# Performance work log

Hardware: AMD Instinct MI355X
Metric: run time of the kernel (lower is better)

## Reference

```python
import math
import jax, jax.numpy as jnp
import numpy as np

B, H, S, D = 2, 16, 2048, 64

def setup_inputs() -> dict:
    key = jax.random.key(0)
    kq, kk, kv, km = jax.random.split(key, 4)
    q = jax.random.normal(kq, (B, H, S, D), dtype=jnp.float32)
    k = jax.random.normal(kk, (B, H, S, D), dtype=jnp.float32)
    v = jax.random.normal(kv, (B, H, S, D), dtype=jnp.float32)
    mask = jax.random.randint(km, (B, S, S), 0, 2, dtype=jnp.int32)
    return {"q": q, "k": k, "v": v, "mask": mask}

def reference(q, k, v, mask):
    # attn = q @ (k^T / sqrt(d))  -> [B,H,Sq,Sk]
    scale = 1.0 / math.sqrt(q.shape[-1])
    attn = jnp.einsum("bhqd,bhkd->bhqk", q, k * scale)
    # masked_fill where mask.unsqueeze(1) == 1
    attn = jnp.where(mask[:, None, :, :] == 1, jnp.float32(-1e9), attn)
    attn = jax.nn.softmax(attn, axis=-1)
    # dropout is identity in eval / p=0
    res = jnp.einsum("bhqk,bhkd->bhqd", attn, v)
    return (res, attn)
```

## Files before the change

### kernel.cpp

```cpp
#include <hip/hip_runtime.h>

#define B_ 2
#define H_ 16
#define S_ 2048
#define D_ 64
#define QB 64
#define KT 64
#define NTHREADS 512

typedef _Float16 f16;
typedef _Float16 f16x8 __attribute__((ext_vector_type(8)));
typedef _Float16 f16x4 __attribute__((ext_vector_type(4)));
typedef _Float16 f16x2 __attribute__((ext_vector_type(2)));
typedef float f32x4 __attribute__((ext_vector_type(4)));

#define MFMA16(a, b, c) __builtin_amdgcn_mfma_f32_16x16x32_f16(a, b, c, 0, 0, 0)

__global__ __launch_bounds__(NTHREADS)
void attn_kernel(const float* __restrict__ q, const float* __restrict__ k,
                 const float* __restrict__ v, const int* __restrict__ mask,
                 float* __restrict__ out)
{
    __shared__ f16 Qsh[QB][D_ + 8];
    __shared__ f16 Ksh[KT][D_ + 8];
    __shared__ f16 Vsh[KT][D_ + 2];
    __shared__ f16 Psh[QB][KT + 8];
    __shared__ float rowred[QB];
    __shared__ float rlsh[QB];

    const int tid  = threadIdx.x;
    const int wave = tid >> 6;
    const int lane = tid & 63;
    const int quad = lane >> 4;
    const int l16  = lane & 15;
    const int qi   = wave & 3;
    const int ni   = wave >> 2;

    const int qb = blockIdx.x;
    const int h  = blockIdx.y;
    const int b  = blockIdx.z;
    const int bh = b * H_ + h;

    const float* Qg = q + ((size_t)bh * S_ + (size_t)qb * QB) * D_;
    const float* Kg = k + (size_t)bh * S_ * D_;
    const float* Vg = v + (size_t)bh * S_ * D_;
    const int*   Mg = mask + ((size_t)b * S_ + (size_t)qb * QB) * S_;
    float* res_out  = out + ((size_t)bh * S_ + (size_t)qb * QB) * D_;
    float* attn_out = out + (size_t)B_ * H_ * S_ * D_
                          + ((size_t)bh * S_ + (size_t)qb * QB) * S_;

    if (tid < QB) rowred[tid] = 0.f;

    {
        const int row = tid >> 3;
        const int c   = (tid & 7) * 8;
        const float4 q0 = *(const float4*)(Qg + row * D_ + c);
        const float4 q1 = *(const float4*)(Qg + row * D_ + c + 4);
        f16x8 o;
        o[0] = (f16)(q0.x * 0.125f); o[1] = (f16)(q0.y * 0.125f);
        o[2] = (f16)(q0.z * 0.125f); o[3] = (f16)(q0.w * 0.125f);
        o[4] = (f16)(q1.x * 0.125f); o[5] = (f16)(q1.y * 0.125f);
        o[6] = (f16)(q1.z * 0.125f); o[7] = (f16)(q1.w * 0.125f);
        *(f16x8*)&Qsh[row][c] = o;
    }
    __syncthreads();

    const int qrow0 = qi * 16 + quad * 4;
    const f16x8 a0 = *(const f16x8*)&Qsh[qi * 16 + l16][quad * 8];
    const f16x8 a1 = *(const f16x8*)&Qsh[qi * 16 + l16][32 + quad * 8];

    const int colbase = ni * 16 + l16;
    const int* mp0 = Mg + (size_t)qrow0 * S_ + colbase;

    const int skk = tid >> 3;
    const int sd0 = (tid & 7) * 8;

    float psum[4] = {0.f, 0.f, 0.f, 0.f};
    for (int kt = 0; kt < S_ / KT; ++kt) {
        {
            const float* src = Kg + ((size_t)(kt * KT + skk)) * D_ + sd0;
            const float4 x0 = *(const float4*)(src);
            const float4 x1 = *(const float4*)(src + 4);
            f16x8 o;
            o[0] = (f16)x0.x; o[1] = (f16)x0.y; o[2] = (f16)x0.z; o[3] = (f16)x0.w;
            o[4] = (f16)x1.x; o[5] = (f16)x1.y; o[6] = (f16)x1.z; o[7] = (f16)x1.w;
            *(f16x8*)&Ksh[skk][sd0] = o;
        }
        __syncthreads();
        const f16x8 b0a = *(const f16x8*)&Ksh[colbase][quad * 8];
        const f16x8 b0b = *(const f16x8*)&Ksh[colbase][32 + quad * 8];
        const f16x8 b1a = *(const f16x8*)&Ksh[32 + colbase][quad * 8];
        const f16x8 b1b = *(const f16x8*)&Ksh[32 + colbase][32 + quad * 8];
        f32x4 c0 = {0.f, 0.f, 0.f, 0.f};
        c0 = MFMA16(a0, b0a, c0);
        c0 = MFMA16(a1, b0b, c0);
        f32x4 c1 = {0.f, 0.f, 0.f, 0.f};
        c1 = MFMA16(a0, b1a, c1);
        c1 = MFMA16(a1, b1b, c1);
        const int* mp = mp0 + kt * KT;
#pragma unroll
        for (int r = 0; r < 4; ++r) {
            const int m0 = mp[(size_t)r * S_];
            const int m1 = mp[(size_t)r * S_ + 32];
            psum[r] += (m0 == 1) ? 0.f : __expf(c0[r]);
            psum[r] += (m1 == 1) ? 0.f : __expf(c1[r]);
        }
        __syncthreads();
    }

#pragma unroll
    for (int r = 0; r < 4; ++r) {
        psum[r] += __shfl_xor(psum[r], 1);
        psum[r] += __shfl_xor(psum[r], 2);
        psum[r] += __shfl_xor(psum[r], 4);
        psum[r] += __shfl_xor(psum[r], 8);
    }
    if (l16 == 0) {
#pragma unroll
        for (int r = 0; r < 4; ++r) atomicAdd(&rowred[qrow0 + r], psum[r]);
    }
    __syncthreads();
    if (tid < QB) rlsh[tid] = 1.0f / rowred[tid];
    __syncthreads();
    float rlq[4];
#pragma unroll
    for (int r = 0; r < 4; ++r) rlq[r] = rlsh[qrow0 + r];

    f32x4 oaccA = {0.f, 0.f, 0.f, 0.f};
    f32x4 oaccB = {0.f, 0.f, 0.f, 0.f};
    float* ap0 = attn_out + (size_t)qrow0 * S_ + colbase;

    for (int kt = 0; kt < S_ / KT; ++kt) {
        {
            const float* srck = Kg + ((size_t)(kt * KT + skk)) * D_ + sd0;
            const float4 x0 = *(const float4*)(srck);
            const float4 x1 = *(const float4*)(srck + 4);
            f16x8 o;
            o[0] = (f16)x0.x; o[1] = (f16)x0.y; o[2] = (f16)x0.z; o[3] = (f16)x0.w;
            o[4] = (f16)x1.x; o[5] = (f16)x1.y; o[6] = (f16)x1.z; o[7] = (f16)x1.w;
            *(f16x8*)&Ksh[skk][sd0] = o;

            const float* srcv = Vg + ((size_t)(kt * KT + skk)) * D_ + sd0;
            const float4 y0 = *(const float4*)(srcv);
            const float4 y1 = *(const float4*)(srcv + 4);
            f16x2 p01, p23, p45, p67;
            p01[0] = (f16)y0.x; p01[1] = (f16)y0.y;
            p23[0] = (f16)y0.z; p23[1] = (f16)y0.w;
            p45[0] = (f16)y1.x; p45[1] = (f16)y1.y;
            p67[0] = (f16)y1.z; p67[1] = (f16)y1.w;
            *(f16x2*)&Vsh[skk][sd0]     = p01;
            *(f16x2*)&Vsh[skk][sd0 + 2] = p23;
            *(f16x2*)&Vsh[skk][sd0 + 4] = p45;
            *(f16x2*)&Vsh[skk][sd0 + 6] = p67;
        }
        __syncthreads();
        const f16x8 b0a = *(const f16x8*)&Ksh[colbase][quad * 8];
        const f16x8 b0b = *(const f16x8*)&Ksh[colbase][32 + quad * 8];
        const f16x8 b1a = *(const f16x8*)&Ksh[32 + colbase][quad * 8];
        const f16x8 b1b = *(const f16x8*)&Ksh[32 + colbase][32 + quad * 8];
        f32x4 c0 = {0.f, 0.f, 0.f, 0.f};
        c0 = MFMA16(a0, b0a, c0);
        c0 = MFMA16(a1, b0b, c0);
        f32x4 c1 = {0.f, 0.f, 0.f, 0.f};
        c1 = MFMA16(a0, b1a, c1);
        c1 = MFMA16(a1, b1b, c1);
        const int* mp = mp0 + kt * KT;
        float* ap = ap0 + kt * KT;
#pragma unroll
        for (int r = 0; r < 4; ++r) {
            const int m0 = mp[(size_t)r * S_];
            const int m1 = mp[(size_t)r * S_ + 32];
            const float e0 = (m0 == 1) ? 0.f : __expf(c0[r]);
            const float e1 = (m1 == 1) ? 0.f : __expf(c1[r]);
            const float p0 = e0 * rlq[r];
            const float p1 = e1 * rlq[r];
            ap[(size_t)r * S_]      = p0;
            ap[(size_t)r * S_ + 32] = p1;
            Psh[qrow0 + r][colbase]      = (f16)p0;
            Psh[qrow0 + r][colbase + 32] = (f16)p1;
        }
        __syncthreads();
        const f16x8 pa0 = *(const f16x8*)&Psh[qi * 16 + l16][quad * 8];
        const f16x8 pa1 = *(const f16x8*)&Psh[qi * 16 + l16][32 + quad * 8];
        f16x8 vb0a, vb1a, vb0b, vb1b;
        const int dcolA = colbase;
        const int dcolB = colbase + 32;
#pragma unroll
        for (int j = 0; j < 8; ++j) {
            vb0a[j] = Vsh[quad * 8 + j][dcolA];
            vb1a[j] = Vsh[32 + quad * 8 + j][dcolA];
            vb0b[j] = Vsh[quad * 8 + j][dcolB];
            vb1b[j] = Vsh[32 + quad * 8 + j][dcolB];
        }
        oaccA = MFMA16(pa0, vb0a, oaccA);
        oaccA = MFMA16(pa1, vb1a, oaccA);
        oaccB = MFMA16(pa0, vb0b, oaccB);
        oaccB = MFMA16(pa1, vb1b, oaccB);
        __syncthreads();
    }

#pragma unroll
    for (int r = 0; r < 4; ++r) {
        res_out[(size_t)(qrow0 + r) * D_ + colbase]      = oaccA[r];
        res_out[(size_t)(qrow0 + r) * D_ + colbase + 32] = oaccB[r];
    }
}

extern "C" void kernel_launch(void* const* d_in, const int* in_sizes, int n_in,
                              void* d_out, int out_size, void* d_ws, size_t ws_size,
                              hipStream_t stream) {
    (void)in_sizes; (void)n_in; (void)out_size; (void)d_ws; (void)ws_size;
    const float* q   = (const float*)d_in[0];
    const float* k   = (const float*)d_in[1];
    const float* v   = (const float*)d_in[2];
    const int*  mask = (const int*)d_in[3];
    float* out = (float*)d_out;
    dim3 grid(S_ / QB, H_, B_);
    attn_kernel<<<grid, dim3(NTHREADS), 0, stream>>>(q, k, v, mask, out);
}
```

Baseline: 836.7 us.

## Prefetch next K/V tile and mask into registers during compute

```diff
diff --git a/kernel.cpp b/kernel.cpp
--- a/kernel.cpp
+++ b/kernel.cpp
@@ -6,25 +6,33 @@
 #define D_ 64
 #define QB 64
 #define KT 64
+#define NT (S_ / KT)
 #define NTHREADS 512
+#define KP 4
 
 typedef _Float16 f16;
 typedef _Float16 f16x8 __attribute__((ext_vector_type(8)));
-typedef _Float16 f16x4 __attribute__((ext_vector_type(4)));
 typedef _Float16 f16x2 __attribute__((ext_vector_type(2)));
 typedef float f32x4 __attribute__((ext_vector_type(4)));
 
 #define MFMA16(a, b, c) __builtin_amdgcn_mfma_f32_16x16x32_f16(a, b, c, 0, 0, 0)
 
-__global__ __launch_bounds__(NTHREADS)
+__device__ __forceinline__ f16x8 pack8(const float4 x0, const float4 x1) {
+    f16x8 o;
+    o[0] = (f16)x0.x; o[1] = (f16)x0.y; o[2] = (f16)x0.z; o[3] = (f16)x0.w;
+    o[4] = (f16)x1.x; o[5] = (f16)x1.y; o[6] = (f16)x1.z; o[7] = (f16)x1.w;
+    return o;
+}
+
+__global__ __launch_bounds__(NTHREADS, 8)
 void attn_kernel(const float* __restrict__ q, const float* __restrict__ k,
                  const float* __restrict__ v, const int* __restrict__ mask,
                  float* __restrict__ out)
 {
-    __shared__ f16 Qsh[QB][D_ + 8];
-    __shared__ f16 Ksh[KT][D_ + 8];
+    __shared__ f16 Qsh[QB][D_ + KP];
+    __shared__ f16 Ksh[KT][D_ + KP];
     __shared__ f16 Vsh[KT][D_ + 2];
-    __shared__ f16 Psh[QB][KT + 8];
+    __shared__ f16 Psh[QB][KT + KP];
     __shared__ float rowred[QB];
     __shared__ float rlsh[QB];
 
@@ -75,18 +83,35 @@
     const int skk = tid >> 3;
     const int sd0 = (tid & 7) * 8;
 
+    f16x8 kf;
+    int mcur[8];
+    {
+        const float* src = Kg + (size_t)skk * D_ + sd0;
+        kf = pack8(*(const float4*)src, *(const float4*)(src + 4));
+#pragma unroll
+        for (int r = 0; r < 4; ++r) {
+            mcur[2 * r]     = mp0[(size_t)r * S_];
+            mcur[2 * r + 1] = mp0[(size_t)r * S_ + 32];
+        }
+    }
+
     float psum[4] = {0.f, 0.f, 0.f, 0.f};
-    for (int kt = 0; kt < S_ / KT; ++kt) {
-        {
-            const float* src = Kg + ((size_t)(kt * KT + skk)) * D_ + sd0;
-            const float4 x0 = *(const float4*)(src);
-            const float4 x1 = *(const float4*)(src + 4);
-            f16x8 o;
-            o[0] = (f16)x0.x; o[1] = (f16)x0.y; o[2] = (f16)x0.z; o[3] = (f16)x0.w;
-            o[4] = (f16)x1.x; o[5] = (f16)x1.y; o[6] = (f16)x1.z; o[7] = (f16)x1.w;
-            *(f16x8*)&Ksh[skk][sd0] = o;
-        }
-        __syncthreads();
+    for (int kt = 0; kt < NT; ++kt) {
+        *(f16x8*)&Ksh[skk][sd0] = kf;
+        __syncthreads();
+
+        const int ktn = (kt + 1 < NT) ? kt + 1 : kt;
+        const float* srcn = Kg + ((size_t)(ktn * KT + skk)) * D_ + sd0;
+        const float4 x0 = *(const float4*)(srcn);
+        const float4 x1 = *(const float4*)(srcn + 4);
+        int mnext[8];
+        const int* mpn = mp0 + ktn * KT;
+#pragma unroll
+        for (int r = 0; r < 4; ++r) {
+            mnext[2 * r]     = mpn[(size_t)r * S_];
+            mnext[2 * r + 1] = mpn[(size_t)r * S_ + 32];
+        }
+
         const f16x8 b0a = *(const f16x8*)&Ksh[colbase][quad * 8];
         const f16x8 b0b = *(const f16x8*)&Ksh[colbase][32 + quad * 8];
         const f16x8 b1a = *(const f16x8*)&Ksh[32 + colbase][quad * 8];
@@ -97,14 +122,15 @@
         f32x4 c1 = {0.f, 0.f, 0.f, 0.f};
         c1 = MFMA16(a0, b1a, c1);
         c1 = MFMA16(a1, b1b, c1);
-        const int* mp = mp0 + kt * KT;
-#pragma unroll
-        for (int r = 0; r < 4; ++r) {
-            const int m0 = mp[(size_t)r * S_];
-            const int m1 = mp[(size_t)r * S_ + 32];
-            psum[r] += (m0 == 1) ? 0.f : __expf(c0[r]);
-            psum[r] += (m1 == 1) ? 0.f : __expf(c1[r]);
-        }
+#pragma unroll
+        for (int r = 0; r < 4; ++r) {
+            psum[r] += (mcur[2 * r]     == 1) ? 0.f : __expf(c0[r]);
+            psum[r] += (mcur[2 * r + 1] == 1) ? 0.f : __expf(c1[r]);
+        }
+
+        kf = pack8(x0, x1);
+#pragma unroll
+        for (int r = 0; r < 8; ++r) mcur[r] = mnext[r];
         __syncthreads();
     }
 
@@ -126,34 +152,51 @@
 #pragma unroll
     for (int r = 0; r < 4; ++r) rlq[r] = rlsh[qrow0 + r];
 
+    f16x2 vf0, vf1, vf2, vf3;
+    {
+        const float* srck = Kg + (size_t)skk * D_ + sd0;
+        kf = pack8(*(const float4*)srck, *(const float4*)(srck + 4));
+        const float* srcv = Vg + (size_t)skk * D_ + sd0;
+        const float4 y0 = *(const float4*)(srcv);
+        const float4 y1 = *(const float4*)(srcv + 4);
+        vf0[0] = (f16)y0.x; vf0[1] = (f16)y0.y;
+        vf1[0] = (f16)y0.z; vf1[1] = (f16)y0.w;
+        vf2[0] = (f16)y1.x; vf2[1] = (f16)y1.y;
+        vf3[0] = (f16)y1.z; vf3[1] = (f16)y1.w;
+#pragma unroll
+        for (int r = 0; r < 4; ++r) {
+            mcur[2 * r]     = mp0[(size_t)r * S_];
+            mcur[2 * r + 1] = mp0[(size_t)r * S_ + 32];
+        }
+    }
+
     f32x4 oaccA = {0.f, 0.f, 0.f, 0.f};
     f32x4 oaccB = {0.f, 0.f, 0.f, 0.f};
     float* ap0 = attn_out + (size_t)qrow0 * S_ + colbase;
 
-    for (int kt = 0; kt < S_ / KT; ++kt) {
-        {
-            const float* srck = Kg + ((size_t)(kt * KT + skk)) * D_ + sd0;
-            const float4 x0 = *(const float4*)(srck);
-            const float4 x1 = *(const float4*)(srck + 4);
-            f16x8 o;
-            o[0] = (f16)x0.x; o[1] = (f16)x0.y; o[2] = (f16)x0.z; o[3] = (f16)x0.w;
-            o[4] = (f16)x1.x; o[5] = (f16)x1.y; o[6] = (f16)x1.z; o[7] = (f16)x1.w;
-            *(f16x8*)&Ksh[skk][sd0] = o;
-
-            const float* srcv = Vg + ((size_t)(kt * KT + skk)) * D_ + sd0;
-            const float4 y0 = *(const float4*)(srcv);
-            const float4 y1 = *(const float4*)(srcv + 4);
-            f16x2 p01, p23, p45, p67;
-            p01[0] = (f16)y0.x; p01[1] = (f16)y0.y;
-            p23[0] = (f16)y0.z; p23[1] = (f16)y0.w;
-            p45[0] = (f16)y1.x; p45[1] = (f16)y1.y;
-            p67[0] = (f16)y1.z; p67[1] = (f16)y1.w;
-            *(f16x2*)&Vsh[skk][sd0]     = p01;
-            *(f16x2*)&Vsh[skk][sd0 + 2] = p23;
-            *(f16x2*)&Vsh[skk][sd0 + 4] = p45;
-            *(f16x2*)&Vsh[skk][sd0 + 6] = p67;
-        }
-        __syncthreads();
+    for (int kt = 0; kt < NT; ++kt) {
+        *(f16x8*)&Ksh[skk][sd0] = kf;
+        *(f16x2*)&Vsh[skk][sd0]     = vf0;
+        *(f16x2*)&Vsh[skk][sd0 + 2] = vf1;
+        *(f16x2*)&Vsh[skk][sd0 + 4] = vf2;
+        *(f16x2*)&Vsh[skk][sd0 + 6] = vf3;
+        __syncthreads();
+
+        const int ktn = (kt + 1 < NT) ? kt + 1 : kt;
+        const float* srck = Kg + ((size_t)(ktn * KT + skk)) * D_ + sd0;
+        const float4 x0 = *(const float4*)(srck);
+        const float4 x1 = *(const float4*)(srck + 4);
+        const float* srcv = Vg + ((size_t)(ktn * KT + skk)) * D_ + sd0;
+        const float4 y0 = *(const float4*)(srcv);
+        const float4 y1 = *(const float4*)(srcv + 4);
+        int mnext[8];
+        const int* mpn = mp0 + ktn * KT;
+#pragma unroll
+        for (int r = 0; r < 4; ++r) {
+            mnext[2 * r]     = mpn[(size_t)r * S_];
+            mnext[2 * r + 1] = mpn[(size_t)r * S_ + 32];
+        }
+
         const f16x8 b0a = *(const f16x8*)&Ksh[colbase][quad * 8];
         const f16x8 b0b = *(const f16x8*)&Ksh[colbase][32 + quad * 8];
         const f16x8 b1a = *(const f16x8*)&Ksh[32 + colbase][quad * 8];
@@ -164,14 +207,11 @@
         f32x4 c1 = {0.f, 0.f, 0.f, 0.f};
         c1 = MFMA16(a0, b1a, c1);
         c1 = MFMA16(a1, b1b, c1);
-        const int* mp = mp0 + kt * KT;
         float* ap = ap0 + kt * KT;
 #pragma unroll
         for (int r = 0; r < 4; ++r) {
-            const int m0 = mp[(size_t)r * S_];
-            const int m1 = mp[(size_t)r * S_ + 32];
-            const float e0 = (m0 == 1) ? 0.f : __expf(c0[r]);
-            const float e1 = (m1 == 1) ? 0.f : __expf(c1[r]);
+            const float e0 = (mcur[2 * r]     == 1) ? 0.f : __expf(c0[r]);
+            const float e1 = (mcur[2 * r + 1] == 1) ? 0.f : __expf(c1[r]);
             const float p0 = e0 * rlq[r];
             const float p1 = e1 * rlq[r];
             ap[(size_t)r * S_]      = p0;
@@ -180,6 +220,7 @@
             Psh[qrow0 + r][colbase + 32] = (f16)p1;
         }
         __syncthreads();
+
         const f16x8 pa0 = *(const f16x8*)&Psh[qi * 16 + l16][quad * 8];
         const f16x8 pa1 = *(const f16x8*)&Psh[qi * 16 + l16][32 + quad * 8];
         f16x8 vb0a, vb1a, vb0b, vb1b;
@@ -196,6 +237,14 @@
         oaccA = MFMA16(pa1, vb1a, oaccA);
         oaccB = MFMA16(pa0, vb0b, oaccB);
         oaccB = MFMA16(pa1, vb1b, oaccB);
+
+        kf = pack8(x0, x1);
+        vf0[0] = (f16)y0.x; vf0[1] = (f16)y0.y;
+        vf1[0] = (f16)y0.z; vf1[1] = (f16)y0.w;
+        vf2[0] = (f16)y1.x; vf2[1] = (f16)y1.y;
+        vf3[0] = (f16)y1.z; vf3[1] = (f16)y1.w;
+#pragma unroll
+        for (int r = 0; r < 8; ++r) mcur[r] = mnext[r];
         __syncthreads();
     }
 
```

Result: slower. 919.3 us (+9.9%).
